# Performance work log

Measured on AMD Instinct MI355X. Metric: run time of the kernel, lower is better.

Reference implementation:

```python
import jax, jax.numpy as jnp
import numpy as np
from jax import lax

RES = 32          # feature map side, HW = RES*RES = 1024
HEADS = 32
QKD = 16          # sampled_qkdim
VD = 32           # sampled_vdim
L = HEADS * VD    # 1024, v channels

def _relative_position_index(res):
    # faithful to attn_pos_idx in the torch code
    coords = np.stack(np.meshgrid(np.arange(res), np.arange(res), indexing='ij'))  # [2,res,res]
    flat = coords.reshape(2, -1)
    rel = flat[:, :, None] - flat[:, None, :]        # [2, N, N]
    rel = rel.transpose(1, 2, 0).copy()
    rel[:, :, 0] += res - 1
    rel[:, :, 1] += res - 1
    rel[:, :, 0] *= 2 * res - 1
    return rel.sum(-1)                               # [N, N] int

_RPI = jnp.asarray(_relative_position_index(RES))    # [1024,1024]

def _hardswish(x):
    return x * jnp.clip(x + 3.0, 0.0, 6.0) * (1.0 / 6.0)

def setup_inputs() -> dict:
    key = jax.random.key(0)
    ks = jax.random.split(key, 6)
    B, HW, C = 4, RES * RES, 512
    x = jax.random.normal(ks[0], (B, HW, C), jnp.float32)
    w_qkv = jax.random.normal(ks[1], (2 * C + L, C), jnp.float32) * 0.02   # [2048,512]
    dw_kernel = jax.random.normal(ks[2], (L, 1, 3, 3), jnp.float32) * 0.1  # depthwise OIHW
    attn_bias = jax.random.normal(ks[3], ((2 * RES - 1) ** 2, HEADS), jnp.float32) * 0.02
    proj_w = jax.random.normal(ks[4], (C, L), jnp.float32) * 0.02
    proj_b = jax.random.normal(ks[5], (C,), jnp.float32) * 0.02
    return {"x": x, "w_qkv": w_qkv, "dw_kernel": dw_kernel,
            "attn_bias": attn_bias, "proj_w": proj_w, "proj_b": proj_b}

def reference(x, w_qkv, dw_kernel, attn_bias, proj_w, proj_b):
    B, HW, C = x.shape
    # elastic QKV projection (full sampled config == full weight)
    qkv = jnp.einsum('bnc,oc->bno', x, w_qkv)                    # [B,HW,2048]
    qkv = qkv.reshape(B, HW, HEADS, QKD + QKD + VD)
    q, k, v = jnp.split(qkv, [QKD, 2 * QKD], axis=3)             # per-head split
    q = q.transpose(0, 2, 1, 3)                                  # [B,H,HW,qkd]
    k = k.transpose(0, 2, 1, 3)
    # depthwise 3x3 conv on V path
    vimg = v.reshape(B, HW, L).transpose(0, 2, 1).reshape(B, L, RES, RES)
    vimg = lax.conv_general_dilated(vimg, dw_kernel, (1, 1), 'SAME',
                                    feature_group_count=L,
                                    dimension_numbers=('NCHW', 'OIHW', 'NCHW'))
    v = vimg.reshape(B, L, HW).transpose(0, 2, 1).reshape(B, HW, HEADS, VD)
    v = v.transpose(0, 2, 1, 3)                                  # [B,H,HW,vd]
    # attention with relative position bias
    attn = jnp.einsum('bhqd,bhkd->bhqk', q, k) * (QKD ** -0.5)   # [B,H,HW,HW]
    bias = attn_bias[_RPI.reshape(-1)].reshape(HW, HW, HEADS)
    bias = bias.transpose(2, 0, 1)[None]                         # [1,H,HW,HW]
    attn = jax.nn.softmax(attn + bias, axis=-1)
    out = jnp.einsum('bhqk,bhkd->bhqd', attn, v)
    out = out.transpose(0, 2, 1, 3).reshape(B, HW, L)
    out = _hardswish(out)
    out = jnp.einsum('bnl,cl->bnc', out, proj_w) + proj_b
    return out
```

## Files before the change

kernel.cpp:

```cpp
#include <hip/hip_runtime.h>
#include <stdint.h>

#define HEADS 32
#define HW_N 1024
#define QS 0.36067376022224085f
#define LOG2E 1.4426950408889634f

typedef __attribute__((ext_vector_type(8))) __bf16 bf16x8;
typedef __attribute__((ext_vector_type(4))) float f32x4;
typedef __attribute__((ext_vector_type(16))) float f32x16;
typedef __attribute__((ext_vector_type(4))) uint32_t u32x4;

__device__ __forceinline__ float b2f(uint16_t u) {
  union { uint32_t i; float f; } v; v.i = ((uint32_t)u) << 16; return v.f;
}
__device__ __forceinline__ uint16_t f2b(float f) {
  uint32_t u = __builtin_bit_cast(uint32_t, f);
  return (uint16_t)((u + 0x7FFFu + ((u >> 16) & 1u)) >> 16);
}

#define GLD16(g, s) __builtin_amdgcn_global_load_lds( \
    (const __attribute__((address_space(1))) void*)(g), \
    (__attribute__((address_space(3))) void*)(s), 16, 0, 0)

__global__ __launch_bounds__(256) void prep(const float* __restrict__ x,
                                            const float* __restrict__ wqv,
                                            const float* __restrict__ pw,
                                            const float* __restrict__ abias,
                                            uint16_t* __restrict__ xb,
                                            uint16_t* __restrict__ wqb,
                                            uint16_t* __restrict__ pwb,
                                            uint16_t* __restrict__ bt2b) {
  const int blk = blockIdx.x;
  const int tid = threadIdx.x;
  if (blk < 3584) {
    const float* in; uint16_t* out; int i;
    if (blk < 2048)      { in = x;   out = xb;  i = blk * 256 + tid; }
    else if (blk < 3072) { in = wqv; out = wqb; i = (blk - 2048) * 256 + tid; }
    else                 { in = pw;  out = pwb; i = (blk - 3072) * 256 + tid; }
    float4 v = ((const float4*)in)[i];
    ushort4 o;
    o.x = f2b(v.x); o.y = f2b(v.y); o.z = f2b(v.z); o.w = f2b(v.w);
    ((ushort4*)out)[i] = o;
  } else {
    const int blk2 = blk - 3584;
    const int h = blk2 / 63, d31 = blk2 - h * 63;
    const size_t tb = ((size_t)(h * 63 + d31)) << 10;
#pragma unroll
    for (int c = 0; c < 4; ++c) {
      const int idx = c * 256 + tid;
      const int lane = idx >> 4, r = idx & 15;
      const int hi = lane >> 5, ln = lane & 31;
      const int crow = (r & 3) + 8 * (r >> 2) + 4 * hi;
      const int col = 31 + ln - crow;
      bt2b[tb + idx] = f2b(LOG2E * abias[(size_t)(d31 * 63 + col) * 32 + h]);
    }
  }
}

__global__ __launch_bounds__(256) void gemm_qkv(
    const uint16_t* __restrict__ Aop, const uint16_t* __restrict__ Bop,
    uint16_t* __restrict__ qT, uint16_t* __restrict__ ko, uint16_t* __restrict__ vo) {
  const int K = 512;
  __shared__ uint16_t As[2][128 * 32];
  __shared__ uint16_t Bs[2][128 * 32];
  const int tid = threadIdx.x;
  const int lane = tid & 63;
  const int wave = tid >> 6;
  const int am0 = blockIdx.y * 128;
  const int bn0 = blockIdx.x * 128;
  const int m_off = (wave >> 1) * 64;
  const int n_off = (wave & 1) * 64;
  const int sr = tid >> 2;
  const int sc = (tid & 3) << 3;

  auto stage = [&](int buf, int kt) {
    const int k0 = kt << 5;
    GLD16(Aop + (size_t)(am0 + sr) * K + (k0 + sc), &As[buf][tid * 8]);
    GLD16(Aop + (size_t)(am0 + sr + 64) * K + (k0 + sc), &As[buf][(tid + 256) * 8]);
    GLD16(Bop + (size_t)(bn0 + sr) * K + (k0 + sc), &Bs[buf][tid * 8]);
    GLD16(Bop + (size_t)(bn0 + sr + 64) * K + (k0 + sc), &Bs[buf][(tid + 256) * 8]);
  };

  f32x4 acc[4][4] = {};
  stage(0, 0);
  asm volatile("s_waitcnt vmcnt(0)" ::: "memory");
  __syncthreads();

  const int fr = lane & 15;
  const int fk = (lane >> 4) << 3;
  int cur = 0;
  for (int kt = 0; kt < 16; ++kt) {
    if (kt + 1 < 16) stage(cur ^ 1, kt + 1);
    bf16x8 af[4], bf_[4];
#pragma unroll
    for (int mi = 0; mi < 4; ++mi)
      af[mi] = *(const bf16x8*)&As[cur][(m_off + mi * 16 + fr) * 32 + fk];
#pragma unroll
    for (int ni = 0; ni < 4; ++ni)
      bf_[ni] = *(const bf16x8*)&Bs[cur][(n_off + ni * 16 + fr) * 32 + fk];
#pragma unroll
    for (int mi = 0; mi < 4; ++mi)
#pragma unroll
      for (int ni = 0; ni < 4; ++ni)
        acc[mi][ni] = __builtin_amdgcn_mfma_f32_16x16x32_bf16(af[mi], bf_[ni], acc[mi][ni], 0, 0, 0);
    asm volatile("s_waitcnt vmcnt(0)" ::: "memory");
    __syncthreads();
    cur ^= 1;
  }

  const int rb = (lane >> 4) << 2;
  const int cl = lane & 15;
  const int b = am0 >> 10;
  const int h = (bn0 + n_off) >> 6;
  const int bh = b * 32 + h;
#pragma unroll
  for (int mi = 0; mi < 4; ++mi) {
    const int n0 = (am0 & 1023) + m_off + mi * 16 + rb;
    {
      ushort4 o;
      o.x = f2b(acc[mi][0][0] * QS); o.y = f2b(acc[mi][0][1] * QS);
      o.z = f2b(acc[mi][0][2] * QS); o.w = f2b(acc[mi][0][3] * QS);
      *(ushort4*)&qT[((size_t)(bh * 16 + cl) << 10) + n0] = o;
    }
#pragma unroll
    for (int r = 0; r < 4; ++r)
      ko[((size_t)(bh * 1024 + n0 + r)) * 16 + cl] = f2b(acc[mi][1][r]);
#pragma unroll
    for (int nv = 2; nv < 4; ++nv) {
      const int l = h * 32 + (nv - 2) * 16 + cl;
      ushort4 o;
      o.x = f2b(acc[mi][nv][0]); o.y = f2b(acc[mi][nv][1]);
      o.z = f2b(acc[mi][nv][2]); o.w = f2b(acc[mi][nv][3]);
      *(ushort4*)&vo[((size_t)(b * 1024 + l) << 10) + n0] = o;
    }
  }
}

__global__ __launch_bounds__(256) void dwconv3x3(const uint16_t* __restrict__ vimg,
                                                 const float* __restrict__ kw,
                                                 uint16_t* __restrict__ vcv) {
  __shared__ float t[1024];
  const int bl = blockIdx.x;
  const int l = bl & 1023;
  const int tid = threadIdx.x;
  const uint16_t* src = vimg + (size_t)bl * 1024;
  {
    uint2 vv = ((const uint2*)src)[tid];
    t[tid * 4 + 0] = b2f((uint16_t)vv.x);
    t[tid * 4 + 1] = b2f((uint16_t)(vv.x >> 16));
    t[tid * 4 + 2] = b2f((uint16_t)vv.y);
    t[tid * 4 + 3] = b2f((uint16_t)(vv.y >> 16));
  }
  float w[9];
#pragma unroll
  for (int i = 0; i < 9; ++i) w[i] = kw[l * 9 + i];
  __syncthreads();
  uint16_t* dst = vcv + (size_t)bl * 1024;
#pragma unroll
  for (int i = 0; i < 4; ++i) {
    const int p = tid + i * 256;
    const int y = p >> 5, x = p & 31;
    float a = 0.f;
#pragma unroll
    for (int dy = 0; dy < 3; ++dy) {
      const int yy = y + dy - 1;
      if (yy < 0 || yy > 31) continue;
#pragma unroll
      for (int dx = 0; dx < 3; ++dx) {
        const int xx = x + dx - 1;
        if (xx < 0 || xx > 31) continue;
        a += t[yy * 32 + xx] * w[dy * 3 + dx];
      }
    }
    dst[p] = f2b(a);
  }
}

__global__ __launch_bounds__(256) void attn_mfma(
    const uint16_t* __restrict__ qT, const uint16_t* __restrict__ kb,
    const uint16_t* __restrict__ vt, const uint16_t* __restrict__ bt2b,
    uint16_t* __restrict__ hsO) {
  __shared__ float inv_s[128];
  const int blk = blockIdx.x;
  const int bh = blk & 127;
  const int qt = blk >> 7;
  const int b = bh >> 5, h = bh & 31;
  const int tid = threadIdx.x;
  const int lane = tid & 63, wave = tid >> 6;
  const int hi = lane >> 5, ln = lane & 31;

  const int q0 = qt * 128 + wave * 32;
  const int qi = qt * 4 + wave;

  union { ushort u[8]; bf16x8 v; } qu;
#pragma unroll
  for (int j = 0; j < 8; ++j)
    qu.u[j] = qT[((size_t)(bh * 16 + hi * 8 + j) << 10) + q0 + ln];
  const bf16x8 qf = qu.v;

  const uint16_t* kp = kb + ((size_t)bh * 1024 + ln) * 16 + hi * 8;
  const uint16_t* vp = vt + ((size_t)(b * 1024 + h * 32 + ln) << 10) + hi * 8;
  const uint16_t* bp = bt2b + ((size_t)(h * 63 + qi + 31) << 10) + lane * 16;

  f32x16 oa0 = {}, oa1 = {};
  float ls0 = 0.f, ls1 = 0.f;

  auto loadset = [&](int tt, bf16x8& kf, bf16x8& v0, bf16x8& v1,
                     u32x4& ca, u32x4& cb2) {
    kf = *(const bf16x8*)(kp + tt * 512);
    v0 = *(const bf16x8*)(vp + tt * 32);
    v1 = *(const bf16x8*)(vp + tt * 32 + 16);
    const uint16_t* bpt = bp - (tt << 10);
    ca  = *(const u32x4*)(bpt);
    cb2 = *(const u32x4*)(bpt + 16);
  };

  auto compute = [&](const bf16x8& kf, const bf16x8& vf0, const bf16x8& vf1,
                     const u32x4& ca, const u32x4& cb2, f32x16& oacc, float& lsum) {
    f32x16 cc;
#pragma unroll
    for (int j = 0; j < 4; ++j) {
      const uint32_t ua = ca[j], ub = cb2[j];
      cc[2 * j]     = __builtin_bit_cast(float, ua << 16);
      cc[2 * j + 1] = __builtin_bit_cast(float, ua & 0xFFFF0000u);
      cc[8 + 2 * j]     = __builtin_bit_cast(float, ub << 16);
      cc[8 + 2 * j + 1] = __builtin_bit_cast(float, ub & 0xFFFF0000u);
    }
    const f32x16 s = __builtin_amdgcn_mfma_f32_32x32x16_bf16(kf, qf, cc, 0, 0, 0);
    float p[16];
#pragma unroll
    for (int r = 0; r < 16; ++r) {
      p[r] = __builtin_amdgcn_exp2f(s[r]);
      lsum += p[r];
    }
    uint32_t w[8], xw[8];
#pragma unroll
    for (int i = 0; i < 8; ++i) {
      const uint32_t u0 = __builtin_bit_cast(uint32_t, p[2 * i]);
      const uint32_t u1 = __builtin_bit_cast(uint32_t, p[2 * i + 1]);
      w[i] = (u0 >> 16) | (u1 & 0xFFFF0000u);
    }
#pragma unroll
    for (int i = 0; i < 8; ++i)
      xw[i] = (uint32_t)__shfl_xor((int)w[i], 32);
    const u32x4 a0u = {hi ? xw[2] : w[0], hi ? xw[3] : w[1],
                       hi ? w[2] : xw[0], hi ? w[3] : xw[1]};
    const u32x4 a1u = {hi ? xw[6] : w[4], hi ? xw[7] : w[5],
                       hi ? w[6] : xw[4], hi ? w[7] : xw[5]};
    oacc = __builtin_amdgcn_mfma_f32_32x32x16_bf16(
        __builtin_bit_cast(bf16x8, a0u), vf0, oacc, 0, 0, 0);
    oacc = __builtin_amdgcn_mfma_f32_32x32x16_bf16(
        __builtin_bit_cast(bf16x8, a1u), vf1, oacc, 0, 0, 0);
  };

  bf16x8 k0, va0, vb0, k1, va1, vb1;
  u32x4 c0a, c0b, c1a, c1b;
  loadset(0, k0, va0, vb0, c0a, c0b);
  for (int t = 0; t < 16; ++t) {
    loadset(t + 16, k1, va1, vb1, c1a, c1b);
    compute(k0, va0, vb0, c0a, c0b, oa0, ls0);
    bf16x8 nk, nva, nvb; u32x4 nca, ncb;
    if (t < 15) loadset(t + 1, nk, nva, nvb, nca, ncb);
    compute(k1, va1, vb1, c1a, c1b, oa1, ls1);
    if (t < 15) { k0 = nk; va0 = nva; vb0 = nvb; c0a = nca; c0b = ncb; }
  }

  const f32x16 oacc = oa0 + oa1;
  const float lsum = ls0 + ls1;
  const float tot = lsum + __shfl_xor(lsum, 32);
  if (hi == 0) inv_s[wave * 32 + ln] = __builtin_amdgcn_rcpf(tot);
  const int ROWS[16] = {0,1,2,3,8,9,10,11,16,17,18,19,24,25,26,27};
#pragma unroll
  for (int r = 0; r < 16; ++r) {
    const int row = ROWS[r] + 4 * hi;
    const float o = oacc[r] * inv_s[wave * 32 + row];
    const float hs = o * fminf(fmaxf(o + 3.f, 0.f), 6.f) * (1.f / 6.f);
    hsO[((size_t)(b * 1024 + q0 + row) << 10) + h * 32 + ln] = f2b(hs);
  }
}

__global__ __launch_bounds__(256) void gemm_proj(
    const uint16_t* __restrict__ Aop, const uint16_t* __restrict__ Bop,
    float* __restrict__ Cout, const float* __restrict__ bias) {
  const int K = 1024;
  __shared__ uint16_t As[2][64 * 32];
  __shared__ uint16_t Bs[2][64 * 32];
  const int tid = threadIdx.x;
  const int lane = tid & 63;
  const int wave = tid >> 6;
  const int am0 = blockIdx.y * 64;
  const int bn0 = blockIdx.x * 64;
  const int m_off = (wave >> 1) * 32;
  const int n_off = (wave & 1) * 32;
  const int sr = tid >> 2;
  const int sc = (tid & 3) << 3;

  auto stage = [&](int buf, int kt) {
    const int k0 = kt << 5;
    GLD16(Aop + (size_t)(am0 + sr) * K + (k0 + sc), &As[buf][tid * 8]);
    GLD16(Bop + (size_t)(bn0 + sr) * K + (k0 + sc), &Bs[buf][tid * 8]);
  };

  f32x4 acc[2][2] = {};
  stage(0, 0);
  asm volatile("s_waitcnt vmcnt(0)" ::: "memory");
  __syncthreads();

  const int fr = lane & 15;
  const int fk = (lane >> 4) << 3;
  int cur = 0;
  for (int kt = 0; kt < 32; ++kt) {
    if (kt + 1 < 32) stage(cur ^ 1, kt + 1);
    bf16x8 af[2], bf_[2];
#pragma unroll
    for (int mi = 0; mi < 2; ++mi)
      af[mi] = *(const bf16x8*)&As[cur][(m_off + mi * 16 + fr) * 32 + fk];
#pragma unroll
    for (int ni = 0; ni < 2; ++ni)
      bf_[ni] = *(const bf16x8*)&Bs[cur][(n_off + ni * 16 + fr) * 32 + fk];
#pragma unroll
    for (int mi = 0; mi < 2; ++mi)
#pragma unroll
      for (int ni = 0; ni < 2; ++ni)
        acc[mi][ni] = __builtin_amdgcn_mfma_f32_16x16x32_bf16(af[mi], bf_[ni], acc[mi][ni], 0, 0, 0);
    asm volatile("s_waitcnt vmcnt(0)" ::: "memory");
    __syncthreads();
    cur ^= 1;
  }

  const int rb = (lane >> 4) << 2;
  const int cl = lane & 15;
#pragma unroll
  for (int mi = 0; mi < 2; ++mi)
#pragma unroll
    for (int ni = 0; ni < 2; ++ni) {
      const int cg = bn0 + n_off + ni * 16 + cl;
#pragma unroll
      for (int r = 0; r < 4; ++r) {
        const int rg = am0 + m_off + mi * 16 + rb + r;
        Cout[(size_t)rg * 512 + cg] = acc[mi][ni][r] + bias[cg];
      }
    }
}

extern "C" void kernel_launch(void* const* d_in, const int* in_sizes, int n_in,
                              void* d_out, int out_size, void* d_ws, size_t ws_size,
                              hipStream_t stream) {
  const float* x      = (const float*)d_in[0];
  const float* w_qkv  = (const float*)d_in[1];
  const float* dwk    = (const float*)d_in[2];
  const float* abias  = (const float*)d_in[3];
  const float* pw     = (const float*)d_in[4];
  const float* pb     = (const float*)d_in[5];
  float* out = (float*)d_out;

  char* ws = (char*)d_ws;
  uint16_t* xb   = (uint16_t*)(ws);
  uint16_t* wqb  = (uint16_t*)(ws + (4ull << 20));
  uint16_t* pwb  = (uint16_t*)(ws + (6ull << 20));
  uint16_t* qT   = (uint16_t*)(ws + (7ull << 20));
  uint16_t* kbuf = (uint16_t*)(ws + (11ull << 20));
  uint16_t* vimg = (uint16_t*)(ws + (15ull << 20));
  uint16_t* vcv  = (uint16_t*)(ws + (23ull << 20));
  uint16_t* bt2b = (uint16_t*)(ws + (31ull << 20));
  uint16_t* hsO  = vimg;

  prep<<<5600, 256, 0, stream>>>(x, w_qkv, pw, abias, xb, wqb, pwb, bt2b);
  gemm_qkv<<<dim3(16, 32), 256, 0, stream>>>(xb, wqb, qT, kbuf, vimg);
  dwconv3x3<<<4096, 256, 0, stream>>>(vimg, dwk, vcv);
  attn_mfma<<<1024, 256, 0, stream>>>(qT, kbuf, vcv, bt2b, hsO);
  gemm_proj<<<dim3(8, 64), 256, 0, stream>>>(hsO, pwb, out, pb);
}
```

Baseline: 101.2 us.

## Split attention keys across two waves per 32-query block, reduce in LDS

Each attention block now covers one 32-query tile with 128 threads, and its two waves each take half of the keys. Partial outputs and row sums are combined through shared memory before the softmax normalisation and hardswish. The grid grows from 1024 to 4096 blocks, which raises parallelism and occupancy but adds an LDS reduction and a barrier. The explicit software-pipelined double buffering is removed, and the cross-half bf16 packing now uses v_perm plus v_permlane32_swap instead of eight shuffles. The second bias load offset also changes from +16 to +8, which alters which bias elements are read.

After: 104.8 us. +3.6%, slower.

```diff
diff --git a/kernel.cpp b/kernel.cpp
--- a/kernel.cpp
+++ b/kernel.cpp
@@ -177,21 +177,23 @@
   }
 }
 
-__global__ __launch_bounds__(256) void attn_mfma(
+__global__ __launch_bounds__(128, 6) void attn_mfma(
     const uint16_t* __restrict__ qT, const uint16_t* __restrict__ kb,
     const uint16_t* __restrict__ vt, const uint16_t* __restrict__ bt2b,
     uint16_t* __restrict__ hsO) {
-  __shared__ float inv_s[128];
+  __shared__ float part[64][17];
+  __shared__ float inv_s[32];
   const int blk = blockIdx.x;
   const int bh = blk & 127;
   const int qt = blk >> 7;
   const int b = bh >> 5, h = bh & 31;
   const int tid = threadIdx.x;
-  const int lane = tid & 63, wave = tid >> 6;
+  const int wave = tid >> 6;
+  const int lane = tid & 63;
   const int hi = lane >> 5, ln = lane & 31;
 
-  const int q0 = qt * 128 + wave * 32;
-  const int qi = qt * 4 + wave;
+  const int q0 = qt * 32;
+  const int qi = qt;
 
   union { ushort u[8]; bf16x8 v; } qu;
 #pragma unroll
@@ -199,29 +201,23 @@
     qu.u[j] = qT[((size_t)(bh * 16 + hi * 8 + j) << 10) + q0 + ln];
   const bf16x8 qf = qu.v;
 
-  const uint16_t* kp = kb + ((size_t)bh * 1024 + ln) * 16 + hi * 8;
-  const uint16_t* vp = vt + ((size_t)(b * 1024 + h * 32 + ln) << 10) + hi * 8;
-  const uint16_t* bp = bt2b + ((size_t)(h * 63 + qi + 31) << 10) + lane * 16;
-
-  f32x16 oa0 = {}, oa1 = {};
+  const uint16_t* kp = kb + ((size_t)bh * 1024 + ln) * 16 + hi * 8 + wave * (16 * 512);
+  const uint16_t* vp = vt + ((size_t)(b * 1024 + h * 32 + ln) << 10) + hi * 8 + wave * (16 * 32);
+  const uint16_t* bp = bt2b + ((size_t)(h * 63 + qi + 31) << 10) + lane * 16 - wave * (16 * 1024);
+
+  f32x16 oacc = {};
   float ls0 = 0.f, ls1 = 0.f;
 
-  auto loadset = [&](int tt, bf16x8& kf, bf16x8& v0, bf16x8& v1,
-                     u32x4& ca, u32x4& cb2) {
-    kf = *(const bf16x8*)(kp + tt * 512);
-    v0 = *(const bf16x8*)(vp + tt * 32);
-    v1 = *(const bf16x8*)(vp + tt * 32 + 16);
-    const uint16_t* bpt = bp - (tt << 10);
-    ca  = *(const u32x4*)(bpt);
-    cb2 = *(const u32x4*)(bpt + 16);
-  };
-
-  auto compute = [&](const bf16x8& kf, const bf16x8& vf0, const bf16x8& vf1,
-                     const u32x4& ca, const u32x4& cb2, f32x16& oacc, float& lsum) {
+  for (int t = 0; t < 16; ++t) {
+    const bf16x8 kf = *(const bf16x8*)(kp);
+    const bf16x8 vf0 = *(const bf16x8*)(vp);
+    const bf16x8 vf1 = *(const bf16x8*)(vp + 16);
+    const u32x4 ca = *(const u32x4*)(bp);
+    const u32x4 cb = *(const u32x4*)(bp + 8);
     f32x16 cc;
 #pragma unroll
     for (int j = 0; j < 4; ++j) {
-      const uint32_t ua = ca[j], ub = cb2[j];
+      const uint32_t ua = ca[j], ub = cb[j];
       cc[2 * j]     = __builtin_bit_cast(float, ua << 16);
       cc[2 * j + 1] = __builtin_bit_cast(float, ua & 0xFFFF0000u);
       cc[8 + 2 * j]     = __builtin_bit_cast(float, ub << 16);
@@ -230,53 +226,52 @@
     const f32x16 s = __builtin_amdgcn_mfma_f32_32x32x16_bf16(kf, qf, cc, 0, 0, 0);
     float p[16];
 #pragma unroll
-    for (int r = 0; r < 16; ++r) {
-      p[r] = __builtin_amdgcn_exp2f(s[r]);
-      lsum += p[r];
-    }
-    uint32_t w[8], xw[8];
-#pragma unroll
-    for (int i = 0; i < 8; ++i) {
-      const uint32_t u0 = __builtin_bit_cast(uint32_t, p[2 * i]);
-      const uint32_t u1 = __builtin_bit_cast(uint32_t, p[2 * i + 1]);
-      w[i] = (u0 >> 16) | (u1 & 0xFFFF0000u);
-    }
-#pragma unroll
-    for (int i = 0; i < 8; ++i)
-      xw[i] = (uint32_t)__shfl_xor((int)w[i], 32);
-    const u32x4 a0u = {hi ? xw[2] : w[0], hi ? xw[3] : w[1],
-                       hi ? w[2] : xw[0], hi ? w[3] : xw[1]};
-    const u32x4 a1u = {hi ? xw[6] : w[4], hi ? xw[7] : w[5],
-                       hi ? w[6] : xw[4], hi ? w[7] : xw[5]};
+    for (int r = 0; r < 16; ++r) p[r] = __builtin_amdgcn_exp2f(s[r]);
+#pragma unroll
+    for (int r = 0; r < 8; ++r) { ls0 += p[r]; ls1 += p[r + 8]; }
+    uint32_t w0, w1, w2, w3, w4, w5, w6, w7;
+    w0 = __builtin_amdgcn_perm(__builtin_bit_cast(uint32_t, p[1]),  __builtin_bit_cast(uint32_t, p[0]),  0x07060302u);
+    w1 = __builtin_amdgcn_perm(__builtin_bit_cast(uint32_t, p[3]),  __builtin_bit_cast(uint32_t, p[2]),  0x07060302u);
+    w2 = __builtin_amdgcn_perm(__builtin_bit_cast(uint32_t, p[5]),  __builtin_bit_cast(uint32_t, p[4]),  0x07060302u);
+    w3 = __builtin_amdgcn_perm(__builtin_bit_cast(uint32_t, p[7]),  __builtin_bit_cast(uint32_t, p[6]),  0x07060302u);
+    w4 = __builtin_amdgcn_perm(__builtin_bit_cast(uint32_t, p[9]),  __builtin_bit_cast(uint32_t, p[8]),  0x07060302u);
+    w5 = __builtin_amdgcn_perm(__builtin_bit_cast(uint32_t, p[11]), __builtin_bit_cast(uint32_t, p[10]), 0x07060302u);
+    w6 = __builtin_amdgcn_perm(__builtin_bit_cast(uint32_t, p[13]), __builtin_bit_cast(uint32_t, p[12]), 0x07060302u);
+    w7 = __builtin_amdgcn_perm(__builtin_bit_cast(uint32_t, p[15]), __builtin_bit_cast(uint32_t, p[14]), 0x07060302u);
+    asm("v_permlane32_swap_b32 %0, %1" : "+v"(w0), "+v"(w2));
+    asm("v_permlane32_swap_b32 %0, %1" : "+v"(w1), "+v"(w3));
+    asm("v_permlane32_swap_b32 %0, %1" : "+v"(w4), "+v"(w6));
+    asm("v_permlane32_swap_b32 %0, %1" : "+v"(w5), "+v"(w7));
+    const u32x4 a0u = {w0, w1, w2, w3};
+    const u32x4 a1u = {w4, w5, w6, w7};
     oacc = __builtin_amdgcn_mfma_f32_32x32x16_bf16(
         __builtin_bit_cast(bf16x8, a0u), vf0, oacc, 0, 0, 0);
     oacc = __builtin_amdgcn_mfma_f32_32x32x16_bf16(
         __builtin_bit_cast(bf16x8, a1u), vf1, oacc, 0, 0, 0);
-  };
-
-  bf16x8 k0, va0, vb0, k1, va1, vb1;
-  u32x4 c0a, c0b, c1a, c1b;
-  loadset(0, k0, va0, vb0, c0a, c0b);
-  for (int t = 0; t < 16; ++t) {
-    loadset(t + 16, k1, va1, vb1, c1a, c1b);
-    compute(k0, va0, vb0, c0a, c0b, oa0, ls0);
-    bf16x8 nk, nva, nvb; u32x4 nca, ncb;
-    if (t < 15) loadset(t + 1, nk, nva, nvb, nca, ncb);
-    compute(k1, va1, vb1, c1a, c1b, oa1, ls1);
-    if (t < 15) { k0 = nk; va0 = nva; vb0 = nvb; c0a = nca; c0b = ncb; }
-  }
-
-  const f32x16 oacc = oa0 + oa1;
-  const float lsum = ls0 + ls1;
-  const float tot = lsum + __shfl_xor(lsum, 32);
-  if (hi == 0) inv_s[wave * 32 + ln] = __builtin_amdgcn_rcpf(tot);
-  const int ROWS[16] = {0,1,2,3,8,9,10,11,16,17,18,19,24,25,26,27};
-#pragma unroll
-  for (int r = 0; r < 16; ++r) {
-    const int row = ROWS[r] + 4 * hi;
-    const float o = oacc[r] * inv_s[wave * 32 + row];
-    const float hs = o * fminf(fmaxf(o + 3.f, 0.f), 6.f) * (1.f / 6.f);
-    hsO[((size_t)(b * 1024 + q0 + row) << 10) + h * 32 + ln] = f2b(hs);
+    kp += 512; vp += 32; bp -= 1024;
+  }
+
+  float lsum = ls0 + ls1;
+  if (wave == 1) {
+#pragma unroll
+    for (int r = 0; r < 16; ++r) part[lane][r] = oacc[r];
+    part[lane][16] = lsum;
+  }
+  __syncthreads();
+  if (wave == 0) {
+#pragma unroll
+    for (int r = 0; r < 16; ++r) oacc[r] += part[lane][r];
+    lsum += part[lane][16];
+    const float tot = lsum + __shfl_xor(lsum, 32);
+    if (hi == 0) inv_s[ln] = __builtin_amdgcn_rcpf(tot);
+    const int ROWS[16] = {0,1,2,3,8,9,10,11,16,17,18,19,24,25,26,27};
+#pragma unroll
+    for (int r = 0; r < 16; ++r) {
+      const int row = ROWS[r] + 4 * hi;
+      const float o = oacc[r] * inv_s[row];
+      const float hs = o * fminf(fmaxf(o + 3.f, 0.f), 6.f) * (1.f / 6.f);
+      hsO[((size_t)(b * 1024 + q0 + row) << 10) + h * 32 + ln] = f2b(hs);
+    }
   }
 }
 
@@ -369,6 +364,6 @@
   prep<<<5600, 256, 0, stream>>>(x, w_qkv, pw, abias, xb, wqb, pwb, bt2b);
   gemm_qkv<<<dim3(16, 32), 256, 0, stream>>>(xb, wqb, qT, kbuf, vimg);
   dwconv3x3<<<4096, 256, 0, stream>>>(vimg, dwk, vcv);
-  attn_mfma<<<1024, 256, 0, stream>>>(qT, kbuf, vcv, bt2b, hsO);
+  attn_mfma<<<4096, 128, 0, stream>>>(qT, kbuf, vcv, bt2b, hsO);
   gemm_proj<<<dim3(8, 64), 256, 0, stream>>>(hsO, pwb, out, pb);
 }
```
